# Performance work log

Hardware: AMD Instinct MI355X
Metric: run time of the kernel (lower is better)

Reference implementation:

```python
import jax, jax.numpy as jnp
from jax import lax
import numpy as np

LRELU_SLOPE = 0.1
DILATIONS = (1, 2, 4)
B, C, T = 8, 256, 8192


def pd_indexing(x, d, dilation):
    """Pitch-dependent past/future gather along time.
    x: (B, C, T); d: (B, 1, T) float dilation factors.
    Returns xP, xF: (B, C, T), zero where index is out of range.
    """
    b, c, t_len = x.shape
    t = jnp.arange(t_len, dtype=x.dtype)  # (T,)
    dil = d[:, 0, :] * dilation           # (B, T)
    idxP = jnp.round(t[None, :] - dil).astype(jnp.int32)  # (B, T)
    idxF = jnp.round(t[None, :] + dil).astype(jnp.int32)  # (B, T)
    validP = (idxP >= 0).astype(x.dtype)[:, None, :]        # (B,1,T)
    validF = (idxF < t_len).astype(x.dtype)[:, None, :]
    idxPc = jnp.broadcast_to(jnp.clip(idxP, 0, t_len - 1)[:, None, :], (b, c, t_len))
    idxFc = jnp.broadcast_to(jnp.clip(idxF, 0, t_len - 1)[:, None, :], (b, c, t_len))
    xP = jnp.take_along_axis(x, idxPc, axis=2) * validP
    xF = jnp.take_along_axis(x, idxFc, axis=2) * validF
    return xP, xF


def conv1x1(x, w, bias):
    # x: (B,C,T), w: (O,C), bias: (O,)
    return jnp.einsum('oc,bct->bot', w, x) + bias[None, :, None]


def conv3(x, w, bias):
    # x: (B,C,T), w: (O,C,3), padding=1
    y = lax.conv_general_dilated(x, w, window_strides=(1,), padding=[(1, 1)],
                                 dimension_numbers=('NCH', 'OIH', 'NCH'))
    return y + bias[None, :, None]


def setup_inputs() -> dict:
    key = jax.random.key(0)
    ks = jax.random.split(key, 8)
    x = jax.random.normal(ks[0], (B, C, T), dtype=jnp.float32)
    d = jax.random.uniform(ks[1], (B, 1, T), dtype=jnp.float32, minval=0.0, maxval=16.0)
    n = len(DILATIONS)
    s1 = 1.0 / np.sqrt(C)
    s3 = 1.0 / np.sqrt(3 * C)
    WC = jax.random.normal(ks[2], (n, C, C), dtype=jnp.float32) * s1
    WP = jax.random.normal(ks[3], (n, C, C), dtype=jnp.float32) * s1
    WF = jax.random.normal(ks[4], (n, C, C), dtype=jnp.float32) * s1
    WA = jax.random.normal(ks[5], (n, C, C, 3), dtype=jnp.float32) * s3
    bC = jnp.zeros((n, C), dtype=jnp.float32)
    bP = jnp.zeros((n, C), dtype=jnp.float32)
    bF = jnp.zeros((n, C), dtype=jnp.float32)
    bA = jnp.zeros((n, C), dtype=jnp.float32)
    return {"x": x, "d": d, "WC": WC, "bC": bC, "WP": WP, "bP": bP,
            "WF": WF, "bF": bF, "WA": WA, "bA": bA}


def reference(x, d, WC, bC, WP, bP, WF, bF, WA, bA):
    for i, dilation in enumerate(DILATIONS):
        xt = jax.nn.leaky_relu(x, LRELU_SLOPE)
        xP, xF = pd_indexing(xt, d, dilation)
        xt = conv1x1(xt, WC[i], bC[i]) + conv1x1(xP, WP[i], bP[i]) + conv1x1(xF, WF[i], bF[i])
        xt = jax.nn.leaky_relu(xt, LRELU_SLOPE)
        xt = conv3(xt, WA[i], bA[i])
        x = xt + x
    return x
```

## Files before the change

### kernel.cpp

```cpp
#include <hip/hip_runtime.h>
#include <hip/hip_bf16.h>
#include <cstddef>
#include <cstdint>

constexpr int Bn = 8, Cn = 256, Tn = 8192;
constexpr int NL = 3;
constexpr int Kc = 768;
constexpr float SLOPE = 0.1f;

typedef unsigned short u16;
using bf8   = __attribute__((ext_vector_type(8))) short;
using f32x4 = __attribute__((ext_vector_type(4))) float;

__device__ __forceinline__ float lrelu(float v) { return v > 0.f ? v : SLOPE * v; }
__device__ __forceinline__ u16 f2bf(float f) {
    __hip_bfloat16 h = __float2bfloat16(f);
    return *reinterpret_cast<u16*>(&h);
}

__device__ __forceinline__ void g2l16(const u16* g, u16* l) {
    __builtin_amdgcn_global_load_lds(
        (const __attribute__((address_space(1))) char*)g,
        (__attribute__((address_space(3))) char*)l, 16, 0, 0);
}

__device__ __forceinline__ void pipe_barrier() {
    __builtin_amdgcn_s_barrier();
    __builtin_amdgcn_sched_barrier(0);
}

__global__ __launch_bounds__(256)
void k_wprep(const float* __restrict__ WC, const float* __restrict__ WP,
             const float* __restrict__ WF, const float* __restrict__ WA,
             const float* __restrict__ bC, const float* __restrict__ bP,
             const float* __restrict__ bF,
             u16* __restrict__ Wcat, u16* __restrict__ WAp, float* __restrict__ bSum,
             u16* __restrict__ zrow)
{
    if (blockIdx.x == 0) zrow[threadIdx.x] = 0;
    const int n1 = NL * Cn * Kc;
    for (int i = blockIdx.x * blockDim.x + threadIdx.x; i < n1;
         i += gridDim.x * blockDim.x) {
        int c = i % Cn;
        int s = (i / Cn) % 3;
        int o = (i / (3 * Cn)) % Cn;
        int l = i / (3 * Cn * Cn);
        size_t src = ((size_t)l * Cn + o) * Cn + c;
        float wc = (s == 0) ? WC[src] : (s == 1) ? WP[src] : WF[src];
        Wcat[i] = f2bf(wc);
        WAp[i] = f2bf(WA[src * 3 + s]);
    }
    for (int i = blockIdx.x * blockDim.x + threadIdx.x; i < NL * Cn;
         i += gridDim.x * blockDim.x)
        bSum[i] = bC[i] + bP[i] + bF[i];
}

__global__ __launch_bounds__(256)
void k_prep(const float* __restrict__ x, u16* __restrict__ xT)
{
    __shared__ float s[64][65];
    const int b = blockIdx.z, c0 = blockIdx.y * 64, t0 = blockIdx.x * 64;
    const int tid = threadIdx.x;
    const float* xb = x + ((size_t)b * Cn + c0) * Tn + t0;

    int tt = tid & 63, c4 = tid >> 6;
    for (int cc = c4; cc < 64; cc += 4)
        s[cc][tt] = xb[(size_t)cc * Tn + tt];
    __syncthreads();

    int ccS = tid & 63, t4 = tid >> 6;
    u16* xTb = xT + ((size_t)b * Tn + t0) * Cn + c0;
    for (int t2 = t4; t2 < 64; t2 += 4)
        xTb[(size_t)t2 * Cn + ccS] = f2bf(lrelu(s[ccS][t2]));
}

__global__ __launch_bounds__(256)
void k_gemm1(const u16* __restrict__ xT, const float* __restrict__ d,
             const u16* __restrict__ Wl, const float* __restrict__ bS,
             float dil, u16* __restrict__ zT, const u16* __restrict__ zrow)
{
    __shared__ u16 smem[8 * 4096];
    __shared__ int sRow[3][128];

    const int tid = threadIdx.x;
    const int b = blockIdx.z;
    const int t0 = blockIdx.x * 128;
    const int o0 = blockIdx.y * 128;

    if (tid < 128) {
        int t = t0 + tid;
        float dv = d[(size_t)b * Tn + t] * dil;
        int ip = (int)rintf((float)t - dv);
        int iF = (int)rintf((float)t + dv);
        sRow[0][tid] = t;
        sRow[1][tid] = (ip >= 0) ? ip : -1;
        sRow[2][tid] = (iF < Tn) ? iF : -1;
    }
    __syncthreads();

    const int srow = tid >> 2;
    const int schunkL = (tid & 3) * 8;
    const int schunkG = ((tid & 3) ^ ((tid >> 3) & 3)) * 8;
    const u16* xTb = xT + (size_t)b * Tn * Cn;

    const u16 *pr0[3], *pr1[3];
    #pragma unroll
    for (int s = 0; s < 3; ++s) {
        int r0 = sRow[s][srow], r1 = sRow[s][srow + 64];
        pr0[s] = (r0 >= 0) ? (xTb + (size_t)r0 * Cn + schunkG) : (zrow + schunkG);
        pr1[s] = (r1 >= 0) ? (xTb + (size_t)r1 * Cn + schunkG) : (zrow + schunkG);
    }
    const u16* wbase = Wl + (size_t)(o0 + srow) * Kc + schunkG;

    const int lane = tid & 63, wv = tid >> 6;
    const int wm = (wv & 1) * 64;
    const int wn = (wv >> 1) * 64;
    const int lr = lane & 15, quad = lane >> 4;
    const int rchunk = (quad ^ ((lr >> 1) & 3)) * 8;

    const int ldsW = srow * 32 + schunkL;
    const int ldsW2 = (srow + 64) * 32 + schunkL;

    auto dma = [&](int kg, int bsel) {
        int seg = kg >> 3, kk = (kg & 7) * 32;
        u16* bx = smem + bsel * 4096;
        u16* bw = smem + 16384 + bsel * 4096;
        g2l16(wbase + seg * 256 + kk,                   bw + ldsW);
        g2l16(wbase + (size_t)64 * Kc + seg * 256 + kk, bw + ldsW2);
        g2l16(pr0[seg] + kk, bx + ldsW);
        g2l16(pr1[seg] + kk, bx + ldsW2);
    };

    f32x4 acc[4][4] = {};
    dma(0, 0); dma(1, 1); dma(2, 2);

    #pragma unroll
    for (int kg = 0; kg < 24; ++kg) {
        if (kg < 22)
            asm volatile("s_waitcnt vmcnt(8) lgkmcnt(0)" ::: "memory");
        else if (kg == 22)
            asm volatile("s_waitcnt vmcnt(4) lgkmcnt(0)" ::: "memory");
        else
            asm volatile("s_waitcnt vmcnt(0) lgkmcnt(0)" ::: "memory");
        pipe_barrier();

        const u16* bX = smem + (kg & 3) * 4096;
        const u16* bW = smem + 16384 + (kg & 3) * 4096;

        bf8 af[4], bg[4];
        #pragma unroll
        for (int mi = 0; mi < 4; ++mi)
            af[mi] = *(const bf8*)(bX + (wm + mi * 16 + lr) * 32 + rchunk);
        #pragma unroll
        for (int ni = 0; ni < 4; ++ni)
            bg[ni] = *(const bf8*)(bW + (wn + ni * 16 + lr) * 32 + rchunk);

        if (kg + 3 < 24) dma(kg + 3, (kg + 3) & 3);

        __builtin_amdgcn_s_setprio(1);
        #pragma unroll
        for (int mi = 0; mi < 4; ++mi)
            #pragma unroll
            for (int ni = 0; ni < 4; ++ni)
                acc[mi][ni] = __builtin_amdgcn_mfma_f32_16x16x32_bf16(
                    af[mi], bg[ni], acc[mi][ni], 0, 0, 0);
        __builtin_amdgcn_s_setprio(0);
    }

    float bias[4];
    #pragma unroll
    for (int ni = 0; ni < 4; ++ni) bias[ni] = bS[o0 + wn + ni * 16 + lr];
    u16* zTb = zT + (size_t)b * Tn * Cn;
    #pragma unroll
    for (int mi = 0; mi < 4; ++mi)
        #pragma unroll
        for (int r = 0; r < 4; ++r) {
            int t = t0 + wm + mi * 16 + quad * 4 + r;
            u16* row = zTb + (size_t)t * Cn + o0 + wn;
            #pragma unroll
            for (int ni = 0; ni < 4; ++ni)
                row[ni * 16 + lr] = f2bf(lrelu(acc[mi][ni][r] + bias[ni]));
        }
}

__global__ __launch_bounds__(256)
void k_gemm2(const u16* __restrict__ zT, const u16* __restrict__ WAl,
             const float* __restrict__ bA, const float* __restrict__ xres,
             float* __restrict__ out, u16* __restrict__ xTn, int writeXT,
             const u16* __restrict__ zrow)
{
    __shared__ u16 smem[8 * 4096];

    const int tid = threadIdx.x;
    const int b = blockIdx.z;
    const int t0 = blockIdx.x * 128;
    const int o0 = blockIdx.y * 128;

    const int srow = tid >> 2;
    const int schunkL = (tid & 3) * 8;
    const int schunkG = ((tid & 3) ^ ((tid >> 3) & 3)) * 8;
    const int lane = tid & 63, wv = tid >> 6;
    const int wo = (wv & 1) * 64;
    const int wt = (wv >> 1) * 64;
    const int lr = lane & 15, quad = lane >> 4;
    const int rchunk = (quad ^ ((lr >> 1) & 3)) * 8;

    const u16* zTb = zT + (size_t)b * Tn * Cn;
    const u16 *zr0[3], *zr1[3];
    #pragma unroll
    for (int tap = 0; tap < 3; ++tap) {
        int r0 = t0 + srow + tap - 1;
        int r1 = r0 + 64;
        zr0[tap] = (r0 >= 0 && r0 < Tn) ? (zTb + (size_t)r0 * Cn + schunkG)
                                        : (zrow + schunkG);
        zr1[tap] = (r1 >= 0 && r1 < Tn) ? (zTb + (size_t)r1 * Cn + schunkG)
                                        : (zrow + schunkG);
    }
    const u16* wbase = WAl + (size_t)(o0 + srow) * Kc + schunkG;

    const int ldsW = srow * 32 + schunkL;
    const int ldsW2 = (srow + 64) * 32 + schunkL;

    auto dma = [&](int kg, int bsel) {
        int tap = kg >> 3, kk = (kg & 7) * 32;
        u16* bz = smem + bsel * 4096;
        u16* bw = smem + 16384 + bsel * 4096;
        g2l16(wbase + tap * 256 + kk,                   bw + ldsW);
        g2l16(wbase + (size_t)64 * Kc + tap * 256 + kk, bw + ldsW2);
        g2l16(zr0[tap] + kk, bz + ldsW);
        g2l16(zr1[tap] + kk, bz + ldsW2);
    };

    f32x4 acc[4][4] = {};
    dma(0, 0); dma(1, 1); dma(2, 2);

    #pragma unroll
    for (int kg = 0; kg < 24; ++kg) {
        if (kg < 22)
            asm volatile("s_waitcnt vmcnt(8) lgkmcnt(0)" ::: "memory");
        else if (kg == 22)
            asm volatile("s_waitcnt vmcnt(4) lgkmcnt(0)" ::: "memory");
        else
            asm volatile("s_waitcnt vmcnt(0) lgkmcnt(0)" ::: "memory");
        pipe_barrier();

        const u16* bZ = smem + (kg & 3) * 4096;
        const u16* bW = smem + 16384 + (kg & 3) * 4096;

        bf8 af[4], bg[4];
        #pragma unroll
        for (int mi = 0; mi < 4; ++mi)
            af[mi] = *(const bf8*)(bW + (wo + mi * 16 + lr) * 32 + rchunk);
        #pragma unroll
        for (int ni = 0; ni < 4; ++ni)
            bg[ni] = *(const bf8*)(bZ + (wt + ni * 16 + lr) * 32 + rchunk);

        if (kg + 3 < 24) dma(kg + 3, (kg + 3) & 3);

        __builtin_amdgcn_s_setprio(1);
        #pragma unroll
        for (int mi = 0; mi < 4; ++mi)
            #pragma unroll
            for (int ni = 0; ni < 4; ++ni)
                acc[mi][ni] = __builtin_amdgcn_mfma_f32_16x16x32_bf16(
                    af[mi], bg[ni], acc[mi][ni], 0, 0, 0);
        __builtin_amdgcn_s_setprio(0);
    }

    float biasv[4][4];
    #pragma unroll
    for (int mi = 0; mi < 4; ++mi) {
        float4 bb = *(const float4*)(bA + o0 + wo + mi * 16 + quad * 4);
        biasv[mi][0] = bb.x; biasv[mi][1] = bb.y; biasv[mi][2] = bb.z; biasv[mi][3] = bb.w;
    }

    if (writeXT) {
        u16* strip = smem + wv * 1152;
        u16* xTb2 = xTn + (size_t)b * Tn * Cn;
        #pragma unroll
        for (int ni = 0; ni < 4; ++ni) {
            __syncthreads();
            #pragma unroll
            for (int mi = 0; mi < 4; ++mi) {
                ushort4 pk;
                #pragma unroll
                for (int r = 0; r < 4; ++r) {
                    int o = o0 + wo + mi * 16 + quad * 4 + r;
                    size_t idx = ((size_t)b * Cn + o) * Tn + t0 + wt + ni * 16 + lr;
                    float v = acc[mi][ni][r] + biasv[mi][r] + xres[idx];
                    out[idx] = v;
                    ((u16*)&pk)[r] = f2bf(lrelu(v));
                }
                *(ushort4*)(strip + lr * 72 + mi * 16 + quad * 4) = pk;
            }
            __syncthreads();
            #pragma unroll
            for (int it = 0; it < 2; ++it) {
                int tt = (lane >> 3) + it * 8;
                uint4 vv = *(const uint4*)(strip + tt * 72 + (lane & 7) * 8);
                *(uint4*)(xTb2 + (size_t)(t0 + wt + ni * 16 + tt) * Cn
                          + o0 + wo + (lane & 7) * 8) = vv;
            }
        }
    } else {
        #pragma unroll
        for (int mi = 0; mi < 4; ++mi)
            #pragma unroll
            for (int r = 0; r < 4; ++r) {
                int o = o0 + wo + mi * 16 + quad * 4 + r;
                size_t base = ((size_t)b * Cn + o) * Tn + t0 + wt;
                #pragma unroll
                for (int ni = 0; ni < 4; ++ni) {
                    size_t idx = base + ni * 16 + lr;
                    out[idx] = acc[mi][ni][r] + biasv[mi][r] + xres[idx];
                }
            }
    }
}

extern "C" void kernel_launch(void* const* d_in, const int* in_sizes, int n_in,
                              void* d_out, int out_size, void* d_ws, size_t ws_size,
                              hipStream_t stream)
{
    const float* x  = (const float*)d_in[0];
    const float* d  = (const float*)d_in[1];
    const float* WC = (const float*)d_in[2];
    const float* bC = (const float*)d_in[3];
    const float* WP = (const float*)d_in[4];
    const float* bP = (const float*)d_in[5];
    const float* WF = (const float*)d_in[6];
    const float* bF = (const float*)d_in[7];
    const float* WA = (const float*)d_in[8];
    const float* bA = (const float*)d_in[9];
    float* out = (float*)d_out;

    char* ws = (char*)d_ws;
    u16*   xT   = (u16*)(ws);
    u16*   zT   = (u16*)(ws + (size_t)Bn * Tn * Cn * 2);
    u16*   Wcat = (u16*)(ws + (size_t)2 * Bn * Tn * Cn * 2);
    u16*   WAp  = Wcat + (size_t)NL * Cn * Kc;
    float* bSum = (float*)(WAp + (size_t)NL * Cn * Kc);
    u16*   zrow = (u16*)(bSum + NL * Cn);

    k_wprep<<<dim3(1024), dim3(256), 0, stream>>>(WC, WP, WF, WA, bC, bP, bF,
                                                  Wcat, WAp, bSum, zrow);

    dim3 gP(Tn / 64, Cn / 64, Bn);
    dim3 gG(Tn / 128, Cn / 128, Bn);
    dim3 blk(256);

    k_prep<<<gP, blk, 0, stream>>>(x, xT);

    const float dils[NL] = {1.f, 2.f, 4.f};
    const float* xcur = x;
    for (int i = 0; i < NL; ++i) {
        k_gemm1<<<gG, blk, 0, stream>>>(xT, d,
                                        Wcat + (size_t)i * Cn * Kc,
                                        bSum + (size_t)i * Cn,
                                        dils[i], zT, zrow);
        k_gemm2<<<gG, blk, 0, stream>>>(zT,
                                        WAp + (size_t)i * Cn * Kc,
                                        bA + (size_t)i * Cn,
                                        xcur, out, xT, (i < NL - 1) ? 1 : 0,
                                        zrow);
        xcur = out;
    }
}
```

Baseline: 373.2 us.

## Shrink GEMM pipelines to three LDS stages and use 32-bit row offsets

```diff
diff --git a/kernel.cpp b/kernel.cpp
--- a/kernel.cpp
+++ b/kernel.cpp
@@ -74,12 +74,12 @@
         xTb[(size_t)t2 * Cn + ccS] = f2bf(lrelu(s[ccS][t2]));
 }
 
-__global__ __launch_bounds__(256)
+__global__ __launch_bounds__(256, 3)
 void k_gemm1(const u16* __restrict__ xT, const float* __restrict__ d,
              const u16* __restrict__ Wl, const float* __restrict__ bS,
              float dil, u16* __restrict__ zT, const u16* __restrict__ zrow)
 {
-    __shared__ u16 smem[8 * 4096];
+    __shared__ u16 smem[6 * 4096];
     __shared__ int sRow[3][128];
 
     const int tid = threadIdx.x;
@@ -102,13 +102,15 @@
     const int schunkL = (tid & 3) * 8;
     const int schunkG = ((tid & 3) ^ ((tid >> 3) & 3)) * 8;
     const u16* xTb = xT + (size_t)b * Tn * Cn;
-
-    const u16 *pr0[3], *pr1[3];
+    const char* xbc = (const char*)xTb;
+    const int zoff = (int)((const char*)(zrow + schunkG) - xbc);
+
+    int offX0[3], offX1[3];
     #pragma unroll
     for (int s = 0; s < 3; ++s) {
         int r0 = sRow[s][srow], r1 = sRow[s][srow + 64];
-        pr0[s] = (r0 >= 0) ? (xTb + (size_t)r0 * Cn + schunkG) : (zrow + schunkG);
-        pr1[s] = (r1 >= 0) ? (xTb + (size_t)r1 * Cn + schunkG) : (zrow + schunkG);
+        offX0[s] = (r0 >= 0) ? (int)(((size_t)r0 * Cn + schunkG) * 2) : zoff;
+        offX1[s] = (r1 >= 0) ? (int)(((size_t)r1 * Cn + schunkG) * 2) : zoff;
     }
     const u16* wbase = Wl + (size_t)(o0 + srow) * Kc + schunkG;
 
@@ -124,28 +126,26 @@
     auto dma = [&](int kg, int bsel) {
         int seg = kg >> 3, kk = (kg & 7) * 32;
         u16* bx = smem + bsel * 4096;
-        u16* bw = smem + 16384 + bsel * 4096;
+        u16* bw = smem + 12288 + bsel * 4096;
         g2l16(wbase + seg * 256 + kk,                   bw + ldsW);
         g2l16(wbase + (size_t)64 * Kc + seg * 256 + kk, bw + ldsW2);
-        g2l16(pr0[seg] + kk, bx + ldsW);
-        g2l16(pr1[seg] + kk, bx + ldsW2);
+        g2l16((const u16*)(xbc + offX0[seg] + kk * 2), bx + ldsW);
+        g2l16((const u16*)(xbc + offX1[seg] + kk * 2), bx + ldsW2);
     };
 
     f32x4 acc[4][4] = {};
-    dma(0, 0); dma(1, 1); dma(2, 2);
+    dma(0, 0); dma(1, 1);
 
     #pragma unroll
     for (int kg = 0; kg < 24; ++kg) {
-        if (kg < 22)
-            asm volatile("s_waitcnt vmcnt(8) lgkmcnt(0)" ::: "memory");
-        else if (kg == 22)
+        if (kg < 23)
             asm volatile("s_waitcnt vmcnt(4) lgkmcnt(0)" ::: "memory");
         else
             asm volatile("s_waitcnt vmcnt(0) lgkmcnt(0)" ::: "memory");
         pipe_barrier();
 
-        const u16* bX = smem + (kg & 3) * 4096;
-        const u16* bW = smem + 16384 + (kg & 3) * 4096;
+        const u16* bX = smem + (kg % 3) * 4096;
+        const u16* bW = smem + 12288 + (kg % 3) * 4096;
 
         bf8 af[4], bg[4];
         #pragma unroll
@@ -155,7 +155,7 @@
         for (int ni = 0; ni < 4; ++ni)
             bg[ni] = *(const bf8*)(bW + (wn + ni * 16 + lr) * 32 + rchunk);
 
-        if (kg + 3 < 24) dma(kg + 3, (kg + 3) & 3);
+        if (kg + 2 < 24) dma(kg + 2, (kg + 2) % 3);
 
         __builtin_amdgcn_s_setprio(1);
         #pragma unroll
@@ -183,13 +183,13 @@
         }
 }
 
-__global__ __launch_bounds__(256)
+__global__ __launch_bounds__(256, 3)
 void k_gemm2(const u16* __restrict__ zT, const u16* __restrict__ WAl,
              const float* __restrict__ bA, const float* __restrict__ xres,
              float* __restrict__ out, u16* __restrict__ xTn, int writeXT,
              const u16* __restrict__ zrow)
 {
-    __shared__ u16 smem[8 * 4096];
+    __shared__ u16 smem[6 * 4096];
 
     const int tid = threadIdx.x;
     const int b = blockIdx.z;
@@ -206,15 +206,18 @@
     const int rchunk = (quad ^ ((lr >> 1) & 3)) * 8;
 
     const u16* zTb = zT + (size_t)b * Tn * Cn;
-    const u16 *zr0[3], *zr1[3];
+    const char* zbc = (const char*)zTb;
+    const int zoff = (int)((const char*)(zrow + schunkG) - zbc);
+
+    int offZ0[3], offZ1[3];
     #pragma unroll
     for (int tap = 0; tap < 3; ++tap) {
         int r0 = t0 + srow + tap - 1;
         int r1 = r0 + 64;
-        zr0[tap] = (r0 >= 0 && r0 < Tn) ? (zTb + (size_t)r0 * Cn + schunkG)
-                                        : (zrow + schunkG);
-        zr1[tap] = (r1 >= 0 && r1 < Tn) ? (zTb + (size_t)r1 * Cn + schunkG)
-                                        : (zrow + schunkG);
+        offZ0[tap] = (r0 >= 0 && r0 < Tn)
+                         ? (int)(((size_t)r0 * Cn + schunkG) * 2) : zoff;
+        offZ1[tap] = (r1 >= 0 && r1 < Tn)
+                         ? (int)(((size_t)r1 * Cn + schunkG) * 2) : zoff;
     }
     const u16* wbase = WAl + (size_t)(o0 + srow) * Kc + schunkG;
 
@@ -224,28 +227,26 @@
     auto dma = [&](int kg, int bsel) {
         int tap = kg >> 3, kk = (kg & 7) * 32;
         u16* bz = smem + bsel * 4096;
-        u16* bw = smem + 16384 + bsel * 4096;
+        u16* bw = smem + 12288 + bsel * 4096;
         g2l16(wbase + tap * 256 + kk,                   bw + ldsW);
         g2l16(wbase + (size_t)64 * Kc + tap * 256 + kk, bw + ldsW2);
-        g2l16(zr0[tap] + kk, bz + ldsW);
-        g2l16(zr1[tap] + kk, bz + ldsW2);
+        g2l16((const u16*)(zbc + offZ0[tap] + kk * 2), bz + ldsW);
+        g2l16((const u16*)(zbc + offZ1[tap] + kk * 2), bz + ldsW2);
     };
 
     f32x4 acc[4][4] = {};
-    dma(0, 0); dma(1, 1); dma(2, 2);
+    dma(0, 0); dma(1, 1);
 
     #pragma unroll
     for (int kg = 0; kg < 24; ++kg) {
-        if (kg < 22)
-            asm volatile("s_waitcnt vmcnt(8) lgkmcnt(0)" ::: "memory");
-        else if (kg == 22)
+        if (kg < 23)
             asm volatile("s_waitcnt vmcnt(4) lgkmcnt(0)" ::: "memory");
         else
             asm volatile("s_waitcnt vmcnt(0) lgkmcnt(0)" ::: "memory");
         pipe_barrier();
 
-        const u16* bZ = smem + (kg & 3) * 4096;
-        const u16* bW = smem + 16384 + (kg & 3) * 4096;
+        const u16* bZ = smem + (kg % 3) * 4096;
+        const u16* bW = smem + 12288 + (kg % 3) * 4096;
 
         bf8 af[4], bg[4];
         #pragma unroll
@@ -255,7 +256,7 @@
         for (int ni = 0; ni < 4; ++ni)
             bg[ni] = *(const bf8*)(bZ + (wt + ni * 16 + lr) * 32 + rchunk);
 
-        if (kg + 3 < 24) dma(kg + 3, (kg + 3) & 3);
+        if (kg + 2 < 24) dma(kg + 2, (kg + 2) % 3);
 
         __builtin_amdgcn_s_setprio(1);
         #pragma unroll
```

Result: slower. 396.8 us (+6.3%).

## Process two K-steps per barrier in GEMM kernels and remap block indices

Applied to the files above, without the earlier changes.

```diff
diff --git a/kernel.cpp b/kernel.cpp
--- a/kernel.cpp
+++ b/kernel.cpp
@@ -74,7 +74,7 @@
         xTb[(size_t)t2 * Cn + ccS] = f2bf(lrelu(s[ccS][t2]));
 }
 
-__global__ __launch_bounds__(256)
+__global__ __launch_bounds__(256, 2)
 void k_gemm1(const u16* __restrict__ xT, const float* __restrict__ d,
              const u16* __restrict__ Wl, const float* __restrict__ bS,
              float dil, u16* __restrict__ zT, const u16* __restrict__ zrow)
@@ -84,8 +84,10 @@
 
     const int tid = threadIdx.x;
     const int b = blockIdx.z;
-    const int t0 = blockIdx.x * 128;
-    const int o0 = blockIdx.y * 128;
+    const int fid = blockIdx.x;
+    const int j = fid >> 3;
+    const int o0 = (j & 1) * 128;
+    const int t0 = ((fid & 7) * 8 + (j >> 1)) * 128;
 
     if (tid < 128) {
         int t = t0 + tid;
@@ -132,38 +134,56 @@
     };
 
     f32x4 acc[4][4] = {};
-    dma(0, 0); dma(1, 1); dma(2, 2);
-
-    #pragma unroll
-    for (int kg = 0; kg < 24; ++kg) {
-        if (kg < 22)
-            asm volatile("s_waitcnt vmcnt(8) lgkmcnt(0)" ::: "memory");
-        else if (kg == 22)
-            asm volatile("s_waitcnt vmcnt(4) lgkmcnt(0)" ::: "memory");
-        else
-            asm volatile("s_waitcnt vmcnt(0) lgkmcnt(0)" ::: "memory");
+    dma(0, 0); dma(1, 1);
+
+    #pragma unroll
+    for (int P = 0; P < 12; ++P) {
+        const int k0 = 2 * P, k1 = 2 * P + 1;
+        asm volatile("s_waitcnt vmcnt(0) lgkmcnt(0)" ::: "memory");
         pipe_barrier();
-
-        const u16* bX = smem + (kg & 3) * 4096;
-        const u16* bW = smem + 16384 + (kg & 3) * 4096;
-
-        bf8 af[4], bg[4];
-        #pragma unroll
-        for (int mi = 0; mi < 4; ++mi)
-            af[mi] = *(const bf8*)(bX + (wm + mi * 16 + lr) * 32 + rchunk);
+        if (P < 11) { dma(k0 + 2, (k0 + 2) & 3); dma(k1 + 2, (k1 + 2) & 3); }
+        __builtin_amdgcn_sched_barrier(0);
+
+        const u16* bX0 = smem + (k0 & 3) * 4096;
+        const u16* bW0 = smem + 16384 + (k0 & 3) * 4096;
+        const u16* bX1 = smem + (k1 & 3) * 4096;
+        const u16* bW1 = smem + 16384 + (k1 & 3) * 4096;
+
+        bf8 a0[4], g0[4], a1[4], g1[4];
+        #pragma unroll
+        for (int mi = 0; mi < 4; ++mi)
+            a0[mi] = *(const bf8*)(bX0 + (wm + mi * 16 + lr) * 32 + rchunk);
         #pragma unroll
         for (int ni = 0; ni < 4; ++ni)
-            bg[ni] = *(const bf8*)(bW + (wn + ni * 16 + lr) * 32 + rchunk);
-
-        if (kg + 3 < 24) dma(kg + 3, (kg + 3) & 3);
-
+            g0[ni] = *(const bf8*)(bW0 + (wn + ni * 16 + lr) * 32 + rchunk);
+        __builtin_amdgcn_sched_barrier(0);
+        #pragma unroll
+        for (int mi = 0; mi < 4; ++mi)
+            a1[mi] = *(const bf8*)(bX1 + (wm + mi * 16 + lr) * 32 + rchunk);
+        #pragma unroll
+        for (int ni = 0; ni < 4; ++ni)
+            g1[ni] = *(const bf8*)(bW1 + (wn + ni * 16 + lr) * 32 + rchunk);
+
+        asm volatile("s_waitcnt lgkmcnt(8)" ::: "memory");
+        __builtin_amdgcn_sched_barrier(0);
         __builtin_amdgcn_s_setprio(1);
         #pragma unroll
         for (int mi = 0; mi < 4; ++mi)
             #pragma unroll
             for (int ni = 0; ni < 4; ++ni)
                 acc[mi][ni] = __builtin_amdgcn_mfma_f32_16x16x32_bf16(
-                    af[mi], bg[ni], acc[mi][ni], 0, 0, 0);
+                    a0[mi], g0[ni], acc[mi][ni], 0, 0, 0);
+        __builtin_amdgcn_s_setprio(0);
+
+        asm volatile("s_waitcnt lgkmcnt(0)" ::: "memory");
+        __builtin_amdgcn_sched_barrier(0);
+        __builtin_amdgcn_s_setprio(1);
+        #pragma unroll
+        for (int mi = 0; mi < 4; ++mi)
+            #pragma unroll
+            for (int ni = 0; ni < 4; ++ni)
+                acc[mi][ni] = __builtin_amdgcn_mfma_f32_16x16x32_bf16(
+                    a1[mi], g1[ni], acc[mi][ni], 0, 0, 0);
         __builtin_amdgcn_s_setprio(0);
     }
 
@@ -183,7 +203,7 @@
         }
 }
 
-__global__ __launch_bounds__(256)
+__global__ __launch_bounds__(256, 2)
 void k_gemm2(const u16* __restrict__ zT, const u16* __restrict__ WAl,
              const float* __restrict__ bA, const float* __restrict__ xres,
              float* __restrict__ out, u16* __restrict__ xTn, int writeXT,
@@ -193,8 +213,10 @@
 
     const int tid = threadIdx.x;
     const int b = blockIdx.z;
-    const int t0 = blockIdx.x * 128;
-    const int o0 = blockIdx.y * 128;
+    const int fid = blockIdx.x;
+    const int j = fid >> 3;
+    const int o0 = (j & 1) * 128;
+    const int t0 = ((fid & 7) * 8 + (j >> 1)) * 128;
 
     const int srow = tid >> 2;
     const int schunkL = (tid & 3) * 8;
@@ -232,38 +254,56 @@
     };
 
     f32x4 acc[4][4] = {};
-    dma(0, 0); dma(1, 1); dma(2, 2);
-
-    #pragma unroll
-    for (int kg = 0; kg < 24; ++kg) {
-        if (kg < 22)
-            asm volatile("s_waitcnt vmcnt(8) lgkmcnt(0)" ::: "memory");
-        else if (kg == 22)
-            asm volatile("s_waitcnt vmcnt(4) lgkmcnt(0)" ::: "memory");
-        else
-            asm volatile("s_waitcnt vmcnt(0) lgkmcnt(0)" ::: "memory");
+    dma(0, 0); dma(1, 1);
+
+    #pragma unroll
+    for (int P = 0; P < 12; ++P) {
+        const int k0 = 2 * P, k1 = 2 * P + 1;
+        asm volatile("s_waitcnt vmcnt(0) lgkmcnt(0)" ::: "memory");
         pipe_barrier();
-
-        const u16* bZ = smem + (kg & 3) * 4096;
-        const u16* bW = smem + 16384 + (kg & 3) * 4096;
-
-        bf8 af[4], bg[4];
-        #pragma unroll
-        for (int mi = 0; mi < 4; ++mi)
-            af[mi] = *(const bf8*)(bW + (wo + mi * 16 + lr) * 32 + rchunk);
+        if (P < 11) { dma(k0 + 2, (k0 + 2) & 3); dma(k1 + 2, (k1 + 2) & 3); }
+        __builtin_amdgcn_sched_barrier(0);
+
+        const u16* bZ0 = smem + (k0 & 3) * 4096;
+        const u16* bW0 = smem + 16384 + (k0 & 3) * 4096;
+        const u16* bZ1 = smem + (k1 & 3) * 4096;
+        const u16* bW1 = smem + 16384 + (k1 & 3) * 4096;
+
+        bf8 a0[4], g0[4], a1[4], g1[4];
+        #pragma unroll
+        for (int mi = 0; mi < 4; ++mi)
+            a0[mi] = *(const bf8*)(bW0 + (wo + mi * 16 + lr) * 32 + rchunk);
         #pragma unroll
         for (int ni = 0; ni < 4; ++ni)
-            bg[ni] = *(const bf8*)(bZ + (wt + ni * 16 + lr) * 32 + rchunk);
-
-        if (kg + 3 < 24) dma(kg + 3, (kg + 3) & 3);
-
+            g0[ni] = *(const bf8*)(bZ0 + (wt + ni * 16 + lr) * 32 + rchunk);
+        __builtin_amdgcn_sched_barrier(0);
+        #pragma unroll
+        for (int mi = 0; mi < 4; ++mi)
+            a1[mi] = *(const bf8*)(bW1 + (wo + mi * 16 + lr) * 32 + rchunk);
+        #pragma unroll
+        for (int ni = 0; ni < 4; ++ni)
+            g1[ni] = *(const bf8*)(bZ1 + (wt + ni * 16 + lr) * 32 + rchunk);
+
+        asm volatile("s_waitcnt lgkmcnt(8)" ::: "memory");
+        __builtin_amdgcn_sched_barrier(0);
         __builtin_amdgcn_s_setprio(1);
         #pragma unroll
         for (int mi = 0; mi < 4; ++mi)
             #pragma unroll
             for (int ni = 0; ni < 4; ++ni)
                 acc[mi][ni] = __builtin_amdgcn_mfma_f32_16x16x32_bf16(
-                    af[mi], bg[ni], acc[mi][ni], 0, 0, 0);
+                    a0[mi], g0[ni], acc[mi][ni], 0, 0, 0);
+        __builtin_amdgcn_s_setprio(0);
+
+        asm volatile("s_waitcnt lgkmcnt(0)" ::: "memory");
+        __builtin_amdgcn_sched_barrier(0);
+        __builtin_amdgcn_s_setprio(1);
+        #pragma unroll
+        for (int mi = 0; mi < 4; ++mi)
+            #pragma unroll
+            for (int ni = 0; ni < 4; ++ni)
+                acc[mi][ni] = __builtin_amdgcn_mfma_f32_16x16x32_bf16(
+                    a1[mi], g1[ni], acc[mi][ni], 0, 0, 0);
         __builtin_amdgcn_s_setprio(0);
     }
 
@@ -346,7 +386,7 @@
                                                   Wcat, WAp, bSum, zrow);
 
     dim3 gP(Tn / 64, Cn / 64, Bn);
-    dim3 gG(Tn / 128, Cn / 128, Bn);
+    dim3 gG(128, 1, Bn);
     dim3 blk(256);
 
     k_prep<<<gP, blk, 0, stream>>>(x, xT);
```

After: 373.6 us. About the same (+0.1%).

## Enlarge GEMM tiles to 256x256 with 512-thread blocks and triple buffering

Applied to the files above, without the earlier changes.

```diff
diff --git a/kernel.cpp b/kernel.cpp
--- a/kernel.cpp
+++ b/kernel.cpp
@@ -74,20 +74,21 @@
         xTb[(size_t)t2 * Cn + ccS] = f2bf(lrelu(s[ccS][t2]));
 }
 
-__global__ __launch_bounds__(256)
+constexpr int SLOTU = 16384;
+
+__global__ __launch_bounds__(512, 2)
 void k_gemm1(const u16* __restrict__ xT, const float* __restrict__ d,
              const u16* __restrict__ Wl, const float* __restrict__ bS,
              float dil, u16* __restrict__ zT, const u16* __restrict__ zrow)
 {
-    __shared__ u16 smem[8 * 4096];
-    __shared__ int sRow[3][128];
+    __shared__ u16 smem[3 * SLOTU];
+    __shared__ int sRow[3][256];
 
     const int tid = threadIdx.x;
     const int b = blockIdx.z;
-    const int t0 = blockIdx.x * 128;
-    const int o0 = blockIdx.y * 128;
-
-    if (tid < 128) {
+    const int t0 = blockIdx.x * 256;
+
+    if (tid < 256) {
         int t = t0 + tid;
         float dv = d[(size_t)b * Tn + t] * dil;
         int ip = (int)rintf((float)t - dv);
@@ -106,60 +107,58 @@
     const u16 *pr0[3], *pr1[3];
     #pragma unroll
     for (int s = 0; s < 3; ++s) {
-        int r0 = sRow[s][srow], r1 = sRow[s][srow + 64];
+        int r0 = sRow[s][srow], r1 = sRow[s][srow + 128];
         pr0[s] = (r0 >= 0) ? (xTb + (size_t)r0 * Cn + schunkG) : (zrow + schunkG);
         pr1[s] = (r1 >= 0) ? (xTb + (size_t)r1 * Cn + schunkG) : (zrow + schunkG);
     }
-    const u16* wbase = Wl + (size_t)(o0 + srow) * Kc + schunkG;
+    const u16* wbase = Wl + (size_t)srow * Kc + schunkG;
 
     const int lane = tid & 63, wv = tid >> 6;
-    const int wm = (wv & 1) * 64;
-    const int wn = (wv >> 1) * 64;
+    const int wt = (wv >> 2) * 128;
+    const int wo = (wv & 3) * 64;
     const int lr = lane & 15, quad = lane >> 4;
     const int rchunk = (quad ^ ((lr >> 1) & 3)) * 8;
 
-    const int ldsW = srow * 32 + schunkL;
-    const int ldsW2 = (srow + 64) * 32 + schunkL;
-
-    auto dma = [&](int kg, int bsel) {
+    const int ldsS = srow * 32 + schunkL;
+    const int ldsS2 = (srow + 128) * 32 + schunkL;
+
+    auto dma = [&](int kg, int slot) {
         int seg = kg >> 3, kk = (kg & 7) * 32;
-        u16* bx = smem + bsel * 4096;
-        u16* bw = smem + 16384 + bsel * 4096;
-        g2l16(wbase + seg * 256 + kk,                   bw + ldsW);
-        g2l16(wbase + (size_t)64 * Kc + seg * 256 + kk, bw + ldsW2);
-        g2l16(pr0[seg] + kk, bx + ldsW);
-        g2l16(pr1[seg] + kk, bx + ldsW2);
+        u16* bx = smem + slot * SLOTU;
+        u16* bw = bx + 8192;
+        g2l16(wbase + seg * 256 + kk,                    bw + ldsS);
+        g2l16(wbase + (size_t)128 * Kc + seg * 256 + kk, bw + ldsS2);
+        g2l16(pr0[seg] + kk, bx + ldsS);
+        g2l16(pr1[seg] + kk, bx + ldsS2);
     };
 
-    f32x4 acc[4][4] = {};
-    dma(0, 0); dma(1, 1); dma(2, 2);
+    f32x4 acc[8][4] = {};
+    dma(0, 0); dma(1, 1);
 
     #pragma unroll
     for (int kg = 0; kg < 24; ++kg) {
-        if (kg < 22)
-            asm volatile("s_waitcnt vmcnt(8) lgkmcnt(0)" ::: "memory");
-        else if (kg == 22)
+        if (kg < 23)
             asm volatile("s_waitcnt vmcnt(4) lgkmcnt(0)" ::: "memory");
         else
             asm volatile("s_waitcnt vmcnt(0) lgkmcnt(0)" ::: "memory");
         pipe_barrier();
 
-        const u16* bX = smem + (kg & 3) * 4096;
-        const u16* bW = smem + 16384 + (kg & 3) * 4096;
-
-        bf8 af[4], bg[4];
-        #pragma unroll
-        for (int mi = 0; mi < 4; ++mi)
-            af[mi] = *(const bf8*)(bX + (wm + mi * 16 + lr) * 32 + rchunk);
+        const u16* bX = smem + (kg % 3) * SLOTU;
+        const u16* bW = bX + 8192;
+
+        bf8 af[8], bg[4];
+        #pragma unroll
+        for (int mi = 0; mi < 8; ++mi)
+            af[mi] = *(const bf8*)(bX + (wt + mi * 16 + lr) * 32 + rchunk);
         #pragma unroll
         for (int ni = 0; ni < 4; ++ni)
-            bg[ni] = *(const bf8*)(bW + (wn + ni * 16 + lr) * 32 + rchunk);
-
-        if (kg + 3 < 24) dma(kg + 3, (kg + 3) & 3);
+            bg[ni] = *(const bf8*)(bW + (wo + ni * 16 + lr) * 32 + rchunk);
+
+        if (kg + 2 < 24) dma(kg + 2, (kg + 2) % 3);
 
         __builtin_amdgcn_s_setprio(1);
         #pragma unroll
-        for (int mi = 0; mi < 4; ++mi)
+        for (int mi = 0; mi < 8; ++mi)
             #pragma unroll
             for (int ni = 0; ni < 4; ++ni)
                 acc[mi][ni] = __builtin_amdgcn_mfma_f32_16x16x32_bf16(
@@ -169,38 +168,37 @@
 
     float bias[4];
     #pragma unroll
-    for (int ni = 0; ni < 4; ++ni) bias[ni] = bS[o0 + wn + ni * 16 + lr];
+    for (int ni = 0; ni < 4; ++ni) bias[ni] = bS[wo + ni * 16 + lr];
     u16* zTb = zT + (size_t)b * Tn * Cn;
     #pragma unroll
-    for (int mi = 0; mi < 4; ++mi)
+    for (int mi = 0; mi < 8; ++mi)
         #pragma unroll
         for (int r = 0; r < 4; ++r) {
-            int t = t0 + wm + mi * 16 + quad * 4 + r;
-            u16* row = zTb + (size_t)t * Cn + o0 + wn;
+            int t = t0 + wt + mi * 16 + quad * 4 + r;
+            u16* row = zTb + (size_t)t * Cn + wo;
             #pragma unroll
             for (int ni = 0; ni < 4; ++ni)
                 row[ni * 16 + lr] = f2bf(lrelu(acc[mi][ni][r] + bias[ni]));
         }
 }
 
-__global__ __launch_bounds__(256)
+__global__ __launch_bounds__(512, 2)
 void k_gemm2(const u16* __restrict__ zT, const u16* __restrict__ WAl,
              const float* __restrict__ bA, const float* __restrict__ xres,
              float* __restrict__ out, u16* __restrict__ xTn, int writeXT,
              const u16* __restrict__ zrow)
 {
-    __shared__ u16 smem[8 * 4096];
+    __shared__ u16 smem[3 * SLOTU];
 
     const int tid = threadIdx.x;
     const int b = blockIdx.z;
-    const int t0 = blockIdx.x * 128;
-    const int o0 = blockIdx.y * 128;
+    const int t0 = blockIdx.x * 256;
 
     const int srow = tid >> 2;
     const int schunkL = (tid & 3) * 8;
     const int schunkG = ((tid & 3) ^ ((tid >> 3) & 3)) * 8;
     const int lane = tid & 63, wv = tid >> 6;
-    const int wo = (wv & 1) * 64;
+    const int wo = (wv & 1) * 128;
     const int wt = (wv >> 1) * 64;
     const int lr = lane & 15, quad = lane >> 4;
     const int rchunk = (quad ^ ((lr >> 1) & 3)) * 8;
@@ -210,56 +208,54 @@
     #pragma unroll
     for (int tap = 0; tap < 3; ++tap) {
         int r0 = t0 + srow + tap - 1;
-        int r1 = r0 + 64;
+        int r1 = r0 + 128;
         zr0[tap] = (r0 >= 0 && r0 < Tn) ? (zTb + (size_t)r0 * Cn + schunkG)
                                         : (zrow + schunkG);
         zr1[tap] = (r1 >= 0 && r1 < Tn) ? (zTb + (size_t)r1 * Cn + schunkG)
                                         : (zrow + schunkG);
     }
-    const u16* wbase = WAl + (size_t)(o0 + srow) * Kc + schunkG;
-
-    const int ldsW = srow * 32 + schunkL;
-    const int ldsW2 = (srow + 64) * 32 + schunkL;
-
-    auto dma = [&](int kg, int bsel) {
+    const u16* wbase = WAl + (size_t)srow * Kc + schunkG;
+
+    const int ldsS = srow * 32 + schunkL;
+    const int ldsS2 = (srow + 128) * 32 + schunkL;
+
+    auto dma = [&](int kg, int slot) {
         int tap = kg >> 3, kk = (kg & 7) * 32;
-        u16* bz = smem + bsel * 4096;
-        u16* bw = smem + 16384 + bsel * 4096;
-        g2l16(wbase + tap * 256 + kk,                   bw + ldsW);
-        g2l16(wbase + (size_t)64 * Kc + tap * 256 + kk, bw + ldsW2);
-        g2l16(zr0[tap] + kk, bz + ldsW);
-        g2l16(zr1[tap] + kk, bz + ldsW2);
+        u16* bz = smem + slot * SLOTU;
+        u16* bw = bz + 8192;
+        g2l16(wbase + tap * 256 + kk,                    bw + ldsS);
+        g2l16(wbase + (size_t)128 * Kc + tap * 256 + kk, bw + ldsS2);
+        g2l16(zr0[tap] + kk, bz + ldsS);
+        g2l16(zr1[tap] + kk, bz + ldsS2);
     };
 
-    f32x4 acc[4][4] = {};
-    dma(0, 0); dma(1, 1); dma(2, 2);
+    f32x4 acc[8][4] = {};
+    dma(0, 0); dma(1, 1);
 
     #pragma unroll
     for (int kg = 0; kg < 24; ++kg) {
-        if (kg < 22)
-            asm volatile("s_waitcnt vmcnt(8) lgkmcnt(0)" ::: "memory");
-        else if (kg == 22)
+        if (kg < 23)
             asm volatile("s_waitcnt vmcnt(4) lgkmcnt(0)" ::: "memory");
         else
             asm volatile("s_waitcnt vmcnt(0) lgkmcnt(0)" ::: "memory");
         pipe_barrier();
 
-        const u16* bZ = smem + (kg & 3) * 4096;
-        const u16* bW = smem + 16384 + (kg & 3) * 4096;
-
-        bf8 af[4], bg[4];
-        #pragma unroll
-        for (int mi = 0; mi < 4; ++mi)
+        const u16* bZ = smem + (kg % 3) * SLOTU;
+        const u16* bW = bZ + 8192;
+
+        bf8 af[8], bg[4];
+        #pragma unroll
+        for (int mi = 0; mi < 8; ++mi)
             af[mi] = *(const bf8*)(bW + (wo + mi * 16 + lr) * 32 + rchunk);
         #pragma unroll
         for (int ni = 0; ni < 4; ++ni)
             bg[ni] = *(const bf8*)(bZ + (wt + ni * 16 + lr) * 32 + rchunk);
 
-        if (kg + 3 < 24) dma(kg + 3, (kg + 3) & 3);
+        if (kg + 2 < 24) dma(kg + 2, (kg + 2) % 3);
 
         __builtin_amdgcn_s_setprio(1);
         #pragma unroll
-        for (int mi = 0; mi < 4; ++mi)
+        for (int mi = 0; mi < 8; ++mi)
             #pragma unroll
             for (int ni = 0; ni < 4; ++ni)
                 acc[mi][ni] = __builtin_amdgcn_mfma_f32_16x16x32_bf16(
@@ -267,54 +263,25 @@
         __builtin_amdgcn_s_setprio(0);
     }
 
-    float biasv[4][4];
-    #pragma unroll
-    for (int mi = 0; mi < 4; ++mi) {
-        float4 bb = *(const float4*)(bA + o0 + wo + mi * 16 + quad * 4);
-        biasv[mi][0] = bb.x; biasv[mi][1] = bb.y; biasv[mi][2] = bb.z; biasv[mi][3] = bb.w;
-    }
-
-    if (writeXT) {
-        u16* strip = smem + wv * 1152;
-        u16* xTb2 = xTn + (size_t)b * Tn * Cn;
+    u16* xTb2 = xTn + (size_t)b * Tn * Cn;
+    #pragma unroll
+    for (int mi = 0; mi < 8; ++mi) {
+        int ob = wo + mi * 16 + quad * 4;
+        float4 bb = *(const float4*)(bA + ob);
         #pragma unroll
         for (int ni = 0; ni < 4; ++ni) {
-            __syncthreads();
-            #pragma unroll
-            for (int mi = 0; mi < 4; ++mi) {
-                ushort4 pk;
-                #pragma unroll
-                for (int r = 0; r < 4; ++r) {
-                    int o = o0 + wo + mi * 16 + quad * 4 + r;
-                    size_t idx = ((size_t)b * Cn + o) * Tn + t0 + wt + ni * 16 + lr;
-                    float v = acc[mi][ni][r] + biasv[mi][r] + xres[idx];
-                    out[idx] = v;
-                    ((u16*)&pk)[r] = f2bf(lrelu(v));
-                }
-                *(ushort4*)(strip + lr * 72 + mi * 16 + quad * 4) = pk;
-            }
-            __syncthreads();
-            #pragma unroll
-            for (int it = 0; it < 2; ++it) {
-                int tt = (lane >> 3) + it * 8;
-                uint4 vv = *(const uint4*)(strip + tt * 72 + (lane & 7) * 8);
-                *(uint4*)(xTb2 + (size_t)(t0 + wt + ni * 16 + tt) * Cn
-                          + o0 + wo + (lane & 7) * 8) = vv;
-            }
-        }
-    } else {
-        #pragma unroll
-        for (int mi = 0; mi < 4; ++mi)
+            int t = t0 + wt + ni * 16 + lr;
+            ushort4 px;
             #pragma unroll
             for (int r = 0; r < 4; ++r) {
-                int o = o0 + wo + mi * 16 + quad * 4 + r;
-                size_t base = ((size_t)b * Cn + o) * Tn + t0 + wt;
-                #pragma unroll
-                for (int ni = 0; ni < 4; ++ni) {
-                    size_t idx = base + ni * 16 + lr;
-                    out[idx] = acc[mi][ni][r] + biasv[mi][r] + xres[idx];
-                }
+                size_t idx = ((size_t)b * Cn + ob + r) * Tn + t;
+                float v = acc[mi][ni][r] + ((const float*)&bb)[r] + xres[idx];
+                out[idx] = v;
+                ((u16*)&px)[r] = f2bf(lrelu(v));
             }
+            if (writeXT)
+                *(ushort4*)(xTb2 + (size_t)t * Cn + ob) = px;
+        }
     }
 }
 
@@ -346,10 +313,10 @@
                                                   Wcat, WAp, bSum, zrow);
 
     dim3 gP(Tn / 64, Cn / 64, Bn);
-    dim3 gG(Tn / 128, Cn / 128, Bn);
-    dim3 blk(256);
-
-    k_prep<<<gP, blk, 0, stream>>>(x, xT);
+    dim3 gG(Tn / 256, 1, Bn);
+    dim3 blk(512);
+
+    k_prep<<<gP, dim3(256), 0, stream>>>(x, xT);
 
     const float dils[NL] = {1.f, 2.f, 4.f};
     const float* xcur = x;
```

After: 397.8 us. 6.6% more time.
